# Optimization experiments

Measured on AMD Instinct MI355X. Metric: run time of the kernel, lower is better.

## Reference

```python
import jax, jax.numpy as jnp
import numpy as np

EMBED_DIM = 1024
NUM_HEADS = 16
HEAD_DIM = EMBED_DIM // NUM_HEADS
MLP_HIDDEN = 4096


def layer_norm(x, gamma, beta, eps=1e-5):
    mu = jnp.mean(x, axis=-1, keepdims=True)
    var = jnp.var(x, axis=-1, keepdims=True)
    return (x - mu) / jnp.sqrt(var + eps) * gamma + beta


def setup_inputs() -> dict:
    key = jax.random.key(0)
    ks = jax.random.split(key, 16)
    d, h = EMBED_DIM, MLP_HIDDEN
    s = 0.02
    inp = {
        "x": jax.random.normal(ks[0], (2, 2048, d), dtype=jnp.float32),
        "ln1_g": jnp.ones((d,), jnp.float32),
        "ln1_b": jnp.zeros((d,), jnp.float32),
        "ln2_g": jnp.ones((d,), jnp.float32),
        "ln2_b": jnp.zeros((d,), jnp.float32),
        "Wq": jax.random.normal(ks[1], (d, d), jnp.float32) * s,
        "bq": jnp.zeros((d,), jnp.float32),
        "Wk": jax.random.normal(ks[2], (d, d), jnp.float32) * s,
        "bk": jnp.zeros((d,), jnp.float32),
        "Wv": jax.random.normal(ks[3], (d, d), jnp.float32) * s,
        "bv": jnp.zeros((d,), jnp.float32),
        "Wo": jax.random.normal(ks[4], (d, d), jnp.float32) * s,
        "bo": jnp.zeros((d,), jnp.float32),
        "W1": jax.random.normal(ks[5], (d, h), jnp.float32) * s,
        "b1": jnp.zeros((h,), jnp.float32),
        "W2": jax.random.normal(ks[6], (h, d), jnp.float32) * s,
        "b2": jnp.zeros((d,), jnp.float32),
    }
    return inp


def reference(x, ln1_g, ln1_b, ln2_g, ln2_b, Wq, bq, Wk, bk, Wv, bv, Wo, bo, W1, b1, W2, b2):
    B, T, C = x.shape
    H, Dh = NUM_HEADS, HEAD_DIM
    # attention branch
    xn = layer_norm(x, ln1_g, ln1_b)
    q = (xn @ Wq + bq).reshape(B, T, H, Dh).transpose(0, 2, 1, 3)  # [B,H,T,Dh]
    k = (xn @ Wk + bk).reshape(B, T, H, Dh).transpose(0, 2, 1, 3)
    v = (xn @ Wv + bv).reshape(B, T, H, Dh).transpose(0, 2, 1, 3)
    scores = jnp.einsum('bhtd,bhsd->bhts', q, k) / jnp.sqrt(jnp.float32(Dh))
    attn = jax.nn.softmax(scores, axis=-1)
    out = jnp.einsum('bhts,bhsd->bhtd', attn, v)
    out = out.transpose(0, 2, 1, 3).reshape(B, T, C)
    x = x + out @ Wo + bo
    # MLP branch
    xn2 = layer_norm(x, ln2_g, ln2_b)
    x = x + jax.nn.relu(xn2 @ W1 + b1) @ W2 + b2
    return x
```

## Files before the change

kernel.cpp:

```cpp
#include <hip/hip_runtime.h>

typedef float f32x4 __attribute__((ext_vector_type(4)));
typedef __bf16 bf16x8 __attribute__((ext_vector_type(8)));

constexpr int TT   = 2048;
constexpr int CC   = 1024;
constexpr int HIDN = 4096;
constexpr int MM   = 4096;
constexpr int NQKV = 3072;

union U84 { uint32_t u[4]; bf16x8 v; };

__device__ inline uint32_t cvt_pk_bf16(float lo, float hi) {
  uint32_t r;
  asm("v_cvt_pk_bf16_f32 %0, %1, %2" : "=v"(r) : "v"(lo), "v"(hi));
  return r;
}
__device__ inline ushort f2bf(float f) { return (ushort)(cvt_pk_bf16(f, 0.f) & 0xffffu); }
__device__ inline float bfbits2f(uint32_t bits) {
  union { uint32_t u; float f; } c; c.u = bits; return c.f;
}
__device__ inline float exp2_fast(float x) {
  float r;
  asm("v_exp_f32 %0, %1" : "=v"(r) : "v"(x));
  return r;
}

#define AS1C(p) ((__attribute__((address_space(1))) void*)(p))
#define AS3(p)  ((__attribute__((address_space(3))) void*)(p))

__global__ __launch_bounds__(256) void prep_weights(const float* __restrict__ Wq,
                                                    const float* __restrict__ Wk,
                                                    const float* __restrict__ Wv,
                                                    const float* __restrict__ Wo,
                                                    const float* __restrict__ W1,
                                                    const float* __restrict__ W2,
                                                    const float* __restrict__ bq,
                                                    const float* __restrict__ bk,
                                                    const float* __restrict__ bv,
                                                    const float* __restrict__ x,
                                                    const float* __restrict__ g1,
                                                    const float* __restrict__ b1v,
                                                    ushort* __restrict__ WqkvT,
                                                    ushort* __restrict__ WoT,
                                                    ushort* __restrict__ W1T,
                                                    ushort* __restrict__ W2T,
                                                    float* __restrict__ Bqkv,
                                                    ushort* __restrict__ Xn) {
  const int id = blockIdx.x;
  const int t = threadIdx.x;
  if (id >= 12300) {
    const int row = id - 12300;
    float4 v = reinterpret_cast<const float4*>(x + (size_t)row * CC)[t];
    float s  = v.x + v.y + v.z + v.w;
    float ss = v.x * v.x + v.y * v.y + v.z * v.z + v.w * v.w;
#pragma unroll
    for (int off = 32; off; off >>= 1) {
      s  += __shfl_down(s, off);
      ss += __shfl_down(ss, off);
    }
    __shared__ float red[16];
    const int wid = t >> 6, lane = t & 63;
    if (lane == 0) { red[wid] = s; red[8 + wid] = ss; }
    __syncthreads();
    if (t == 0) {
      red[0] = red[0] + red[1] + red[2] + red[3];
      red[8] = red[8] + red[9] + red[10] + red[11];
    }
    __syncthreads();
    const float mu   = red[0] * (1.0f / CC);
    const float var  = red[8] * (1.0f / CC) - mu * mu;
    const float rstd = rsqrtf(var + 1e-5f);
    float4 gg = reinterpret_cast<const float4*>(g1)[t];
    float4 bb = reinterpret_cast<const float4*>(b1v)[t];
    uint2 st;
    st.x = cvt_pk_bf16((v.x - mu) * rstd * gg.x + bb.x, (v.y - mu) * rstd * gg.y + bb.y);
    st.y = cvt_pk_bf16((v.z - mu) * rstd * gg.z + bb.z, (v.w - mu) * rstd * gg.w + bb.w);
    *reinterpret_cast<uint2*>(Xn + (size_t)row * CC + t * 4) = st;
    return;
  }
  if (id >= 12288) {
    const int i = (id - 12288) * 256 + t;
    Bqkv[i] = (i < 1024) ? bq[i] : ((i < 2048) ? bk[i - 1024] : bv[i - 2048]);
    return;
  }
  const float* W; ushort* out; int Kd, Nd, bx, by, rowOff = 0;
  if (id < 4096) {
    const int which = id >> 10, sub = id & 1023;
    bx = sub & 31; by = sub >> 5; Kd = 1024; Nd = 1024;
    if (which == 0)      { W = Wq; out = WqkvT; rowOff = 0; }
    else if (which == 1) { W = Wk; out = WqkvT; rowOff = 1024; }
    else if (which == 2) { W = Wv; out = WqkvT; rowOff = 2048; }
    else                 { W = Wo; out = WoT; }
  } else if (id < 8192) {
    const int sub = id - 4096; bx = sub & 127; by = sub >> 7;
    W = W1; out = W1T; Kd = 1024; Nd = 4096;
  } else {
    const int sub = id - 8192; bx = sub & 31; by = sub >> 5;
    W = W2; out = W2T; Kd = 4096; Nd = 1024;
  }
  const int n0 = bx * 32, k0 = by * 32;
  __shared__ float Ts[32][33];
  {
    const int r = t >> 3, cb = (t & 7) * 4;
    float4 v = *reinterpret_cast<const float4*>(W + (size_t)(k0 + r) * Nd + n0 + cb);
    Ts[r][cb + 0] = v.x; Ts[r][cb + 1] = v.y; Ts[r][cb + 2] = v.z; Ts[r][cb + 3] = v.w;
  }
  __syncthreads();
  {
    const int nl = t >> 3, kb = (t & 7) * 4;
    uint2 st;
    st.x = cvt_pk_bf16(Ts[kb + 0][nl], Ts[kb + 1][nl]);
    st.y = cvt_pk_bf16(Ts[kb + 2][nl], Ts[kb + 3][nl]);
    *reinterpret_cast<uint2*>(out + (size_t)(rowOff + n0 + nl) * Kd + k0 + kb) = st;
  }
}

template <bool RELU, bool VOUT, bool PARTIAL>
__global__ __launch_bounds__(512, 2) void gemm_8w(const ushort* __restrict__ A,
                                                  const ushort* __restrict__ Bt,
                                                  const float* __restrict__ bias,
                                                  ushort* __restrict__ outp,
                                                  ushort* __restrict__ Vt,
                                                  ushort* __restrict__ P1,
                                                  ushort* __restrict__ P2,
                                                  ushort* __restrict__ P3,
                                                  int N, int K, int Kchunk) {
  __shared__ ushort lds[65536];
  const int t = threadIdx.x, lane = t & 63, w = t >> 6;
  const int g = lane >> 4, i16 = lane & 15;
  const int wr = w >> 2, wc = w & 3;
  const int nwg  = gridDim.x * gridDim.y;
  const int orig = blockIdx.y * gridDim.x + blockIdx.x;
  const int sw   = (orig & 7) * (nwg >> 3) + (orig >> 3);
  const int row0 = (sw / gridDim.x) * 256, col0 = (sw % gridDim.x) * 256;
  const int kstart = PARTIAL ? blockIdx.z * Kchunk : 0;
  const int NT = (PARTIAL ? Kchunk : K) >> 6;
  ushort* __restrict__ Out = outp;
  if (PARTIAL) Out = (blockIdx.z == 0) ? outp : (blockIdx.z == 1) ? P1
              : (blockIdx.z == 2) ? P2 : P3;

  const ushort* aG[4];
  const ushort* bG[4];
#pragma unroll
  for (int i = 0; i < 4; ++i) {
    const int c = t + 512 * i;
    const int r = c >> 3, ssw = (c & 7) ^ (r & 7);
    aG[i] = A  + (size_t)(row0 + r) * K + kstart + ssw * 8;
    bG[i] = Bt + (size_t)(col0 + r) * K + kstart + ssw * 8;
  }

  int aoff[8][2], boff[4][2];
#pragma unroll
  for (int mf = 0; mf < 8; ++mf) {
    const int R = wr * 128 + mf * 16 + i16;
#pragma unroll
    for (int kk = 0; kk < 2; ++kk)
      aoff[mf][kk] = R * 128 + (((kk << 2) | g) ^ (R & 7)) * 16;
  }
#pragma unroll
  for (int nf = 0; nf < 4; ++nf) {
    const int Cn = wc * 64 + nf * 16 + i16;
#pragma unroll
    for (int kk = 0; kk < 2; ++kk)
      boff[nf][kk] = Cn * 128 + (((kk << 2) | g) ^ (Cn & 7)) * 16;
  }

  f32x4 acc[8][4] = {};

  auto STAGE = [&](int bi, int kt) {
    char* aB = (char*)lds + bi * 65536;
    char* bB = aB + 32768;
    const int ko = kt * 64;
#pragma unroll
    for (int i = 0; i < 4; ++i)
      __builtin_amdgcn_global_load_lds(AS1C(aG[i] + ko), AS3(aB + i * 8192 + w * 1024), 16, 0, 0);
#pragma unroll
    for (int i = 0; i < 4; ++i)
      __builtin_amdgcn_global_load_lds(AS1C(bG[i] + ko), AS3(bB + i * 8192 + w * 1024), 16, 0, 0);
  };

  STAGE(0, 0);

  for (int kt = 0; kt < NT; ++kt) {
    const int cur = kt & 1;
    if (kt + 1 < NT) {
      STAGE(cur ^ 1, kt + 1);
      asm volatile("s_waitcnt vmcnt(8)" ::: "memory");
    } else {
      asm volatile("s_waitcnt vmcnt(0)" ::: "memory");
    }
    asm volatile("s_barrier" ::: "memory");
    __builtin_amdgcn_sched_barrier(0);

    const char* aB = (const char*)lds + cur * 65536;
    const char* bB = aB + 32768;
    bf16x8 b4[4][2], a4[4][2];
#pragma unroll
    for (int nf = 0; nf < 4; ++nf)
#pragma unroll
      for (int kk = 0; kk < 2; ++kk)
        b4[nf][kk] = *reinterpret_cast<const bf16x8*>(bB + boff[nf][kk]);
#pragma unroll
    for (int mf = 0; mf < 4; ++mf)
#pragma unroll
      for (int kk = 0; kk < 2; ++kk)
        a4[mf][kk] = *reinterpret_cast<const bf16x8*>(aB + aoff[mf][kk]);
    __builtin_amdgcn_s_setprio(1);
#pragma unroll
    for (int mf = 0; mf < 4; ++mf)
#pragma unroll
      for (int nf = 0; nf < 4; ++nf)
#pragma unroll
        for (int kk = 0; kk < 2; ++kk)
          acc[mf][nf] = __builtin_amdgcn_mfma_f32_16x16x32_bf16(a4[mf][kk], b4[nf][kk], acc[mf][nf], 0, 0, 0);
    __builtin_amdgcn_s_setprio(0);
    asm volatile("s_barrier" ::: "memory");
    __builtin_amdgcn_sched_barrier(0);
#pragma unroll
    for (int mf = 0; mf < 4; ++mf)
#pragma unroll
      for (int kk = 0; kk < 2; ++kk)
        a4[mf][kk] = *reinterpret_cast<const bf16x8*>(aB + aoff[mf + 4][kk]);
    __builtin_amdgcn_s_setprio(1);
#pragma unroll
    for (int mf = 0; mf < 4; ++mf)
#pragma unroll
      for (int nf = 0; nf < 4; ++nf)
#pragma unroll
        for (int kk = 0; kk < 2; ++kk)
          acc[mf + 4][nf] = __builtin_amdgcn_mfma_f32_16x16x32_bf16(a4[mf][kk], b4[nf][kk], acc[mf + 4][nf], 0, 0, 0);
    __builtin_amdgcn_s_setprio(0);
    asm volatile("s_barrier" ::: "memory");
    __builtin_amdgcn_sched_barrier(0);
  }

  const int qcol0 = col0 + wc * 64;

  if (VOUT && qcol0 >= 2048) {
#pragma unroll
    for (int nf = 0; nf < 4; ++nf) {
      const int ncol = qcol0 + nf * 16 + i16;
      const float bb = bias[ncol];
      const int d = ncol - 2048;
      const int hh = d >> 6, dd = d & 63;
#pragma unroll
      for (int mf = 0; mf < 8; ++mf) {
        const int mrow = row0 + wr * 128 + mf * 16 + 4 * g;
        const int bb_ = mrow >> 11, tok = mrow & 2047;
        uint2 st;
        st.x = cvt_pk_bf16(acc[mf][nf][0] + bb, acc[mf][nf][1] + bb);
        st.y = cvt_pk_bf16(acc[mf][nf][2] + bb, acc[mf][nf][3] + bb);
        *reinterpret_cast<uint2*>(Vt + (size_t)((bb_ * 16 + hh) * 64 + dd) * TT + tok) = st;
      }
    }
    return;
  }

  float* Lf = (float*)((char*)lds + w * 4096);
  const int rr2 = lane >> 2, q = lane & 3;
#pragma unroll
  for (int mf = 0; mf < 8; ++mf) {
#pragma unroll
    for (int nf = 0; nf < 4; ++nf)
#pragma unroll
      for (int r = 0; r < 4; ++r) {
        const int row = 4 * g + r;
        Lf[row * 64 + ((16 * nf + i16) ^ ((row & 7) << 2))] = acc[mf][nf][r];
      }
    asm volatile("s_waitcnt lgkmcnt(0)" ::: "memory");
    uint32_t u[8];
#pragma unroll
    for (int j = 0; j < 4; ++j) {
      f32x4 v = *reinterpret_cast<const f32x4*>(Lf + rr2 * 64 + ((q * 16 + 4 * j) ^ ((rr2 & 7) << 2)));
      float e0 = v[0], e1 = v[1], e2 = v[2], e3 = v[3];
      if (!PARTIAL) {
        const float4 b4v = *reinterpret_cast<const float4*>(bias + qcol0 + q * 16 + 4 * j);
        e0 += b4v.x; e1 += b4v.y; e2 += b4v.z; e3 += b4v.w;
        if (RELU) {
          e0 = fmaxf(e0, 0.f); e1 = fmaxf(e1, 0.f);
          e2 = fmaxf(e2, 0.f); e3 = fmaxf(e3, 0.f);
        }
      }
      u[2 * j + 0] = cvt_pk_bf16(e0, e1);
      u[2 * j + 1] = cvt_pk_bf16(e2, e3);
    }
    const int mrow = row0 + wr * 128 + mf * 16 + rr2;
    ushort* orow = Out + (size_t)mrow * N + qcol0 + q * 16;
    uint4 s0; s0.x = u[0]; s0.y = u[1]; s0.z = u[2]; s0.w = u[3];
    uint4 s1; s1.x = u[4]; s1.y = u[5]; s1.z = u[6]; s1.w = u[7];
    *reinterpret_cast<uint4*>(orow) = s0;
    *reinterpret_cast<uint4*>(orow + 8) = s1;
    asm volatile("s_waitcnt lgkmcnt(0)" ::: "memory");
  }
}

__global__ __launch_bounds__(256) void gemm_splitk(const ushort* __restrict__ A,
                                                   const ushort* __restrict__ Bt,
                                                   ushort* __restrict__ P0,
                                                   ushort* __restrict__ P1,
                                                   ushort* __restrict__ P2,
                                                   ushort* __restrict__ P3,
                                                   int N, int K, int Kchunk) {
  __shared__ ushort Smem[8192];
  ushort* Asm = Smem;
  ushort* Bsm = Smem + 4096;
  const int t = threadIdx.x;
  const int lane = t & 63, w = t >> 6;
  const int g = lane >> 4, i16 = lane & 15;
  const int wrow = w >> 1, wcol = w & 1;
  const int nwg  = gridDim.x * gridDim.y;
  const int orig = blockIdx.y * gridDim.x + blockIdx.x;
  const int sw   = (orig & 7) * (nwg >> 3) + (orig >> 3);
  const int row0 = (sw / gridDim.x) * 128, col0 = (sw % gridDim.x) * 128;
  const int kstart = blockIdx.z * Kchunk;
  ushort* __restrict__ P = (blockIdx.z == 0) ? P0 : (blockIdx.z == 1) ? P1
                          : (blockIdx.z == 2) ? P2 : P3;

  f32x4 acc[4][4] = {};

  const int srow = t >> 2, sc = (t & 3) * 8;
  const ushort* aS1 = A + (size_t)(row0 + srow) * K + sc;
  const ushort* aS2 = A + (size_t)(row0 + 64 + srow) * K + sc;
  const ushort* bS1 = Bt + (size_t)(col0 + srow) * K + sc;
  const ushort* bS2 = Bt + (size_t)(col0 + 64 + srow) * K + sc;
  char* aL1 = (char*)Asm + w * 1024;
  char* aL2 = (char*)Asm + 4096 + w * 1024;
  char* bL1 = (char*)Bsm + w * 1024;
  char* bL2 = (char*)Bsm + 4096 + w * 1024;

  for (int k0 = kstart; k0 < kstart + Kchunk; k0 += 32) {
    __syncthreads();
    __builtin_amdgcn_global_load_lds(AS1C(aS1 + k0), AS3(aL1), 16, 0, 0);
    __builtin_amdgcn_global_load_lds(AS1C(aS2 + k0), AS3(aL2), 16, 0, 0);
    __builtin_amdgcn_global_load_lds(AS1C(bS1 + k0), AS3(bL1), 16, 0, 0);
    __builtin_amdgcn_global_load_lds(AS1C(bS2 + k0), AS3(bL2), 16, 0, 0);
    __syncthreads();

    bf16x8 a4[4], b4[4];
#pragma unroll
    for (int mf = 0; mf < 4; ++mf) {
      const int r = wrow * 64 + mf * 16 + i16;
      a4[mf] = *reinterpret_cast<const bf16x8*>((const char*)Asm + r * 64 + g * 16);
    }
#pragma unroll
    for (int nf = 0; nf < 4; ++nf) {
      const int c = wcol * 64 + nf * 16 + i16;
      b4[nf] = *reinterpret_cast<const bf16x8*>((const char*)Bsm + c * 64 + g * 16);
    }
#pragma unroll
    for (int mf = 0; mf < 4; ++mf)
#pragma unroll
      for (int nf = 0; nf < 4; ++nf)
        acc[mf][nf] = __builtin_amdgcn_mfma_f32_16x16x32_bf16(a4[mf], b4[nf], acc[mf][nf], 0, 0, 0);
  }

  __syncthreads();

  float* Lf = (float*)((char*)Smem + w * 4096);
  const int qcol0 = col0 + wcol * 64;
  const int rr = lane >> 2, q = lane & 3;
#pragma unroll
  for (int mf = 0; mf < 4; ++mf) {
#pragma unroll
    for (int nf = 0; nf < 4; ++nf)
#pragma unroll
      for (int r = 0; r < 4; ++r) {
        const int row = 4 * g + r;
        Lf[row * 64 + ((16 * nf + i16) ^ ((row & 7) << 2))] = acc[mf][nf][r];
      }
    asm volatile("s_waitcnt lgkmcnt(0)" ::: "memory");
    uint32_t u[8];
#pragma unroll
    for (int j = 0; j < 4; ++j) {
      f32x4 v = *reinterpret_cast<const f32x4*>(Lf + rr * 64 + ((q * 16 + 4 * j) ^ ((rr & 7) << 2)));
      u[2 * j + 0] = cvt_pk_bf16(v[0], v[1]);
      u[2 * j + 1] = cvt_pk_bf16(v[2], v[3]);
    }
    const int mrow = row0 + wrow * 64 + mf * 16 + rr;
    ushort* orow = P + (size_t)mrow * N + qcol0 + q * 16;
    uint4 s0; s0.x = u[0]; s0.y = u[1]; s0.z = u[2]; s0.w = u[3];
    uint4 s1; s1.x = u[4]; s1.y = u[5]; s1.z = u[6]; s1.w = u[7];
    *reinterpret_cast<uint4*>(orow) = s0;
    *reinterpret_cast<uint4*>(orow + 8) = s1;
    asm volatile("s_waitcnt lgkmcnt(0)" ::: "memory");
  }
}

__device__ inline float bfsum4(uint32_t a, uint32_t b, uint32_t c, uint32_t d, bool hi) {
  if (hi) return bfbits2f(a & 0xffff0000u) + bfbits2f(b & 0xffff0000u) +
                 bfbits2f(c & 0xffff0000u) + bfbits2f(d & 0xffff0000u);
  return bfbits2f(a << 16) + bfbits2f(b << 16) + bfbits2f(c << 16) + bfbits2f(d << 16);
}

__global__ __launch_bounds__(256) void reduce_wo_ln(const ushort* __restrict__ P0,
                                                    const ushort* __restrict__ P1,
                                                    const ushort* __restrict__ P2,
                                                    const ushort* __restrict__ P3,
                                                    const float* __restrict__ x,
                                                    const float* __restrict__ bo,
                                                    const float* __restrict__ g,
                                                    const float* __restrict__ b,
                                                    float* __restrict__ X1f,
                                                    ushort* __restrict__ Xn) {
  const int row = blockIdx.x, t = threadIdx.x;
  const size_t off = (size_t)row * CC + t * 4;
  float4 v  = *reinterpret_cast<const float4*>(x + off);
  const uint2 q0 = *reinterpret_cast<const uint2*>(P0 + off);
  const uint2 q1 = *reinterpret_cast<const uint2*>(P1 + off);
  const uint2 q2 = *reinterpret_cast<const uint2*>(P2 + off);
  const uint2 q3 = *reinterpret_cast<const uint2*>(P3 + off);
  float4 bb = reinterpret_cast<const float4*>(bo)[t];
  v.x += bfsum4(q0.x, q1.x, q2.x, q3.x, false) + bb.x;
  v.y += bfsum4(q0.x, q1.x, q2.x, q3.x, true)  + bb.y;
  v.z += bfsum4(q0.y, q1.y, q2.y, q3.y, false) + bb.z;
  v.w += bfsum4(q0.y, q1.y, q2.y, q3.y, true)  + bb.w;
  *reinterpret_cast<float4*>(X1f + off) = v;

  float s  = v.x + v.y + v.z + v.w;
  float ss = v.x * v.x + v.y * v.y + v.z * v.z + v.w * v.w;
#pragma unroll
  for (int o = 32; o; o >>= 1) {
    s  += __shfl_down(s, o);
    ss += __shfl_down(ss, o);
  }
  __shared__ float red[16];
  const int wid = t >> 6, lane = t & 63;
  if (lane == 0) { red[wid] = s; red[8 + wid] = ss; }
  __syncthreads();
  if (t == 0) {
    red[0] = red[0] + red[1] + red[2] + red[3];
    red[8] = red[8] + red[9] + red[10] + red[11];
  }
  __syncthreads();
  const float mu   = red[0] * (1.0f / CC);
  const float var  = red[8] * (1.0f / CC) - mu * mu;
  const float rstd = rsqrtf(var + 1e-5f);
  float4 gg = reinterpret_cast<const float4*>(g)[t];
  float4 lb = reinterpret_cast<const float4*>(b)[t];
  uint2 st;
  st.x = cvt_pk_bf16((v.x - mu) * rstd * gg.x + lb.x, (v.y - mu) * rstd * gg.y + lb.y);
  st.y = cvt_pk_bf16((v.z - mu) * rstd * gg.z + lb.z, (v.w - mu) * rstd * gg.w + lb.w);
  *reinterpret_cast<uint2*>(Xn + off) = st;
}

__global__ __launch_bounds__(256) void reduce_fc2(const ushort* __restrict__ P0,
                                                  const ushort* __restrict__ P1,
                                                  const ushort* __restrict__ P2,
                                                  const ushort* __restrict__ P3,
                                                  const float* __restrict__ X1,
                                                  const float* __restrict__ b2,
                                                  float* __restrict__ out) {
  const int row = blockIdx.x, t = threadIdx.x;
  const size_t off = (size_t)row * CC + t * 4;
  float4 v  = *reinterpret_cast<const float4*>(X1 + off);
  const uint2 q0 = *reinterpret_cast<const uint2*>(P0 + off);
  const uint2 q1 = *reinterpret_cast<const uint2*>(P1 + off);
  const uint2 q2 = *reinterpret_cast<const uint2*>(P2 + off);
  const uint2 q3 = *reinterpret_cast<const uint2*>(P3 + off);
  float4 bb = reinterpret_cast<const float4*>(b2)[t];
  v.x += bfsum4(q0.x, q1.x, q2.x, q3.x, false) + bb.x;
  v.y += bfsum4(q0.x, q1.x, q2.x, q3.x, true)  + bb.y;
  v.z += bfsum4(q0.y, q1.y, q2.y, q3.y, false) + bb.z;
  v.w += bfsum4(q0.y, q1.y, q2.y, q3.y, true)  + bb.w;
  *reinterpret_cast<float4*>(out + off) = v;
}

__global__ __launch_bounds__(512, 4) void attn_full(const ushort* __restrict__ qkv,
                                                    const ushort* __restrict__ Vt,
                                                    ushort* __restrict__ attnb) {
  __shared__ ushort Ks[2][4096];
  __shared__ ushort Vs[2][4096];
  __shared__ uint32_t Ps[8][16][36];
  const int t = threadIdx.x, lane = t & 63, w = t >> 6;
  const int g = lane >> 4, iq = lane & 15;
  const int flat = blockIdx.x;
  const int work = (flat & 7) * 64 + (flat >> 3);
  const int bh = work >> 4;
  const int qt = work & 15;
  const int b = bh >> 4, h = bh & 15;

  bf16x8 qfrag[2];
  {
    const ushort* qrow = qkv + (size_t)(b * TT + qt * 128 + w * 16 + iq) * NQKV + h * 64;
    const float qs = 0.125f * 1.44269504f;
#pragma unroll
    for (int kk = 0; kk < 2; ++kk) {
      uint4 raw = *reinterpret_cast<const uint4*>(qrow + kk * 32 + g * 8);
      uint32_t rr[4] = {raw.x, raw.y, raw.z, raw.w};
      U84 tmp;
#pragma unroll
      for (int c = 0; c < 4; ++c) {
        float lo = bfbits2f(rr[c] << 16) * qs;
        float hi = bfbits2f(rr[c] & 0xffff0000u) * qs;
        tmp.u[c] = cvt_pk_bf16(lo, hi);
      }
      qfrag[kk] = tmp.v;
    }
  }

  const int sr1 = t >> 3, sc1 = t & 7;
  const int csw = (sc1 ^ (sr1 & 7)) * 8;
  const ushort* kbase = qkv + 1024 + h * 64;
  const ushort* vbase = Vt + (size_t)(bh * 64) * TT;

  auto STAGE = [&](int bi, int kt) {
    const size_t tok = (size_t)(b * TT + kt * 64);
    __builtin_amdgcn_global_load_lds(AS1C(kbase + (tok + sr1) * NQKV + csw),
                                     AS3((char*)&Ks[bi][0] + w * 1024), 16, 0, 0);
    __builtin_amdgcn_global_load_lds(AS1C(vbase + (size_t)sr1 * TT + kt * 64 + csw),
                                     AS3((char*)&Vs[bi][0] + w * 1024), 16, 0, 0);
  };

  uint32_t (*pw)[36] = Ps[w];
  const int wsw = (iq & 8) << 1;
  const int xsb = wsw << 2;
  const char* prow = (const char*)&pw[iq][0];

  float lrun = 0.f;
  f32x4 ot[4] = {};

  constexpr int NKT = TT / 64;
  STAGE(0, 0);

  for (int kt = 0; kt < NKT; ++kt) {
    const int cur = kt & 1;
    if (kt + 1 < NKT) {
      STAGE(cur ^ 1, kt + 1);
      asm volatile("s_waitcnt vmcnt(2)" ::: "memory");
    } else {
      asm volatile("s_waitcnt vmcnt(0)" ::: "memory");
    }
    asm volatile("s_barrier" ::: "memory");
    __builtin_amdgcn_sched_barrier(0);
    const char* Kc = (const char*)&Ks[cur][0];
    const char* Vc = (const char*)&Vs[cur][0];

    f32x4 sfr[4] = {};
    __builtin_amdgcn_s_setprio(1);
#pragma unroll
    for (int kk = 0; kk < 2; ++kk)
#pragma unroll
      for (int jf = 0; jf < 4; ++jf) {
        const int row = iq + 16 * jf;
        const int off = row * 128 + ((kk * 64 + g * 16) ^ ((row & 7) << 4));
        bf16x8 a = *reinterpret_cast<const bf16x8*>(Kc + off);
        sfr[jf] = __builtin_amdgcn_mfma_f32_16x16x32_bf16(a, qfrag[kk], sfr[jf], 0, 0, 0);
      }
    __builtin_amdgcn_s_setprio(0);

#pragma unroll
    for (int f = 0; f < 4; ++f) {
      float p0 = exp2_fast(sfr[f][0]);
      float p1 = exp2_fast(sfr[f][1]);
      float p2 = exp2_fast(sfr[f][2]);
      float p3 = exp2_fast(sfr[f][3]);
      lrun += (p0 + p1) + (p2 + p3);
      uint2 st2;
      st2.x = cvt_pk_bf16(p0, p1);
      st2.y = cvt_pk_bf16(p2, p3);
      *reinterpret_cast<uint2*>(&pw[iq][(8 * f + 2 * g) ^ wsw]) = st2;
    }
    asm volatile("s_waitcnt lgkmcnt(0)" ::: "memory");

    __builtin_amdgcn_s_setprio(1);
#pragma unroll
    for (int kk = 0; kk < 2; ++kk) {
      bf16x8 pb = *reinterpret_cast<const bf16x8*>(prow + ((kk * 64 + g * 16) ^ xsb));
#pragma unroll
      for (int df = 0; df < 4; ++df) {
        const int row = iq + 16 * df;
        const int off = row * 128 + ((kk * 64 + g * 16) ^ ((row & 7) << 4));
        bf16x8 a = *reinterpret_cast<const bf16x8*>(Vc + off);
        ot[df] = __builtin_amdgcn_mfma_f32_16x16x32_bf16(a, pb, ot[df], 0, 0, 0);
      }
    }
    __builtin_amdgcn_s_setprio(0);

    asm volatile("s_barrier" ::: "memory");
    __builtin_amdgcn_sched_barrier(0);
  }

  lrun += __shfl_xor(lrun, 16, 64);
  lrun += __shfl_xor(lrun, 32, 64);
  const int grow = b * TT + qt * 128 + w * 16 + iq;
  const float inv = 1.f / lrun;
  ushort* orow = attnb + (size_t)grow * CC + h * 64;
#pragma unroll
  for (int df = 0; df < 4; ++df) {
    uint2 st;
    st.x = cvt_pk_bf16(ot[df][0] * inv, ot[df][1] * inv);
    st.y = cvt_pk_bf16(ot[df][2] * inv, ot[df][3] * inv);
    *reinterpret_cast<uint2*>(orow + df * 16 + g * 4) = st;
  }
}

extern "C" void kernel_launch(void* const* d_in, const int* in_sizes, int n_in,
                              void* d_out, int out_size, void* d_ws, size_t ws_size,
                              hipStream_t stream) {
  const float* x     = (const float*)d_in[0];
  const float* ln1_g = (const float*)d_in[1];
  const float* ln1_b = (const float*)d_in[2];
  const float* ln2_g = (const float*)d_in[3];
  const float* ln2_b = (const float*)d_in[4];
  const float* Wq = (const float*)d_in[5];
  const float* bq = (const float*)d_in[6];
  const float* Wk = (const float*)d_in[7];
  const float* bk = (const float*)d_in[8];
  const float* Wv = (const float*)d_in[9];
  const float* bv = (const float*)d_in[10];
  const float* Wo = (const float*)d_in[11];
  const float* bo = (const float*)d_in[12];
  const float* W1 = (const float*)d_in[13];
  const float* b1 = (const float*)d_in[14];
  const float* W2 = (const float*)d_in[15];
  const float* b2 = (const float*)d_in[16];
  float* out = (float*)d_out;
  char* ws = (char*)d_ws;

  ushort* WqkvT = (ushort*)(ws + 0);
  ushort* WoT   = (ushort*)(ws + 6291456);
  ushort* W1T   = (ushort*)(ws + 8388608);
  ushort* W2T   = (ushort*)(ws + 16777216);
  float*  Bqkv  = (float*) (ws + 25165824);
  ushort* Xn    = (ushort*)(ws + 25178112);
  ushort* Attn  = (ushort*)(ws + 33566720);
  float*  X1f   = (float*) (ws + 41955328);
  ushort* Qkv   = (ushort*)(ws + 58732544);
  ushort* Vtb   = (ushort*)(ws + 83898368);
  ushort* Hid   = (ushort*)(ws + 58732544);
  ushort* WoP0  = (ushort*)(ws + 58732544);
  ushort* WoP1  = (ushort*)(ws + 67121152);
  ushort* WoP2  = (ushort*)(ws + 75509760);
  ushort* WoP3  = (ushort*)(ws + 83898368);
  ushort* F2P0  = (ushort*)(ws + 0);
  ushort* F2P1  = (ushort*)(ws + 8388608);
  ushort* F2P2  = (ushort*)(ws + 25178112);
  ushort* F2P3  = (ushort*)(ws + 33566720);

  const dim3 blk(256);

  prep_weights<<<dim3(16396), blk, 0, stream>>>(Wq, Wk, Wv, Wo, W1, W2, bq, bk, bv,
                                                x, ln1_g, ln1_b,
                                                WqkvT, WoT, W1T, W2T, Bqkv, Xn);
  gemm_8w<false, true, false><<<dim3(12, 16), dim3(512), 0, stream>>>(
      Xn, WqkvT, Bqkv, Qkv, Vtb, nullptr, nullptr, nullptr, NQKV, 1024, 0);
  attn_full<<<dim3(512), dim3(512), 0, stream>>>(Qkv, Vtb, Attn);
  gemm_splitk<<<dim3(8, 32, 4), blk, 0, stream>>>(Attn, WoT, WoP0, WoP1, WoP2, WoP3, 1024, 1024, 256);
  reduce_wo_ln<<<dim3(MM), blk, 0, stream>>>(WoP0, WoP1, WoP2, WoP3, x, bo, ln2_g, ln2_b, X1f, Xn);
  gemm_8w<true, false, false><<<dim3(16, 16), dim3(512), 0, stream>>>(
      Xn, W1T, b1, Hid, nullptr, nullptr, nullptr, nullptr, HIDN, 1024, 0);
  gemm_8w<false, false, true><<<dim3(4, 16, 4), dim3(512), 0, stream>>>(
      Hid, W2T, nullptr, F2P0, nullptr, F2P1, F2P2, F2P3, 1024, 4096, 1024);
  reduce_fc2<<<dim3(MM), blk, 0, stream>>>(F2P0, F2P1, F2P2, F2P3, X1f, b2, out);
}
```

Measured before the change: 234.4 us.

## Split attention over two KV halves with a combine kernel; reuse gemm_8w for Wo

The attention kernel now splits each (batch, head, query-tile) across two halves of the key sequence. This doubles the grid to 1024 workgroups for better CU fill. Each half writes an unnormalized bf16 partial output plus its row sums, and a new combine kernel adds the two partials and normalizes. The Wo projection drops its dedicated 256-thread split-K GEMM and uses the existing 8-wave gemm_8w split-K path. The trade-off is an extra kernel launch, extra memory traffic for the partials, and bf16 rounding of unnormalized partials. The combine also assumes both halves share the same max offset, since no per-half max is stored or rescaled.

Result: no change. 236.1 us (+0.8%).

```diff
diff --git a/kernel.cpp b/kernel.cpp
--- a/kernel.cpp
+++ b/kernel.cpp
@@ -295,98 +295,6 @@
   }
 }
 
-__global__ __launch_bounds__(256) void gemm_splitk(const ushort* __restrict__ A,
-                                                   const ushort* __restrict__ Bt,
-                                                   ushort* __restrict__ P0,
-                                                   ushort* __restrict__ P1,
-                                                   ushort* __restrict__ P2,
-                                                   ushort* __restrict__ P3,
-                                                   int N, int K, int Kchunk) {
-  __shared__ ushort Smem[8192];
-  ushort* Asm = Smem;
-  ushort* Bsm = Smem + 4096;
-  const int t = threadIdx.x;
-  const int lane = t & 63, w = t >> 6;
-  const int g = lane >> 4, i16 = lane & 15;
-  const int wrow = w >> 1, wcol = w & 1;
-  const int nwg  = gridDim.x * gridDim.y;
-  const int orig = blockIdx.y * gridDim.x + blockIdx.x;
-  const int sw   = (orig & 7) * (nwg >> 3) + (orig >> 3);
-  const int row0 = (sw / gridDim.x) * 128, col0 = (sw % gridDim.x) * 128;
-  const int kstart = blockIdx.z * Kchunk;
-  ushort* __restrict__ P = (blockIdx.z == 0) ? P0 : (blockIdx.z == 1) ? P1
-                          : (blockIdx.z == 2) ? P2 : P3;
-
-  f32x4 acc[4][4] = {};
-
-  const int srow = t >> 2, sc = (t & 3) * 8;
-  const ushort* aS1 = A + (size_t)(row0 + srow) * K + sc;
-  const ushort* aS2 = A + (size_t)(row0 + 64 + srow) * K + sc;
-  const ushort* bS1 = Bt + (size_t)(col0 + srow) * K + sc;
-  const ushort* bS2 = Bt + (size_t)(col0 + 64 + srow) * K + sc;
-  char* aL1 = (char*)Asm + w * 1024;
-  char* aL2 = (char*)Asm + 4096 + w * 1024;
-  char* bL1 = (char*)Bsm + w * 1024;
-  char* bL2 = (char*)Bsm + 4096 + w * 1024;
-
-  for (int k0 = kstart; k0 < kstart + Kchunk; k0 += 32) {
-    __syncthreads();
-    __builtin_amdgcn_global_load_lds(AS1C(aS1 + k0), AS3(aL1), 16, 0, 0);
-    __builtin_amdgcn_global_load_lds(AS1C(aS2 + k0), AS3(aL2), 16, 0, 0);
-    __builtin_amdgcn_global_load_lds(AS1C(bS1 + k0), AS3(bL1), 16, 0, 0);
-    __builtin_amdgcn_global_load_lds(AS1C(bS2 + k0), AS3(bL2), 16, 0, 0);
-    __syncthreads();
-
-    bf16x8 a4[4], b4[4];
-#pragma unroll
-    for (int mf = 0; mf < 4; ++mf) {
-      const int r = wrow * 64 + mf * 16 + i16;
-      a4[mf] = *reinterpret_cast<const bf16x8*>((const char*)Asm + r * 64 + g * 16);
-    }
-#pragma unroll
-    for (int nf = 0; nf < 4; ++nf) {
-      const int c = wcol * 64 + nf * 16 + i16;
-      b4[nf] = *reinterpret_cast<const bf16x8*>((const char*)Bsm + c * 64 + g * 16);
-    }
-#pragma unroll
-    for (int mf = 0; mf < 4; ++mf)
-#pragma unroll
-      for (int nf = 0; nf < 4; ++nf)
-        acc[mf][nf] = __builtin_amdgcn_mfma_f32_16x16x32_bf16(a4[mf], b4[nf], acc[mf][nf], 0, 0, 0);
-  }
-
-  __syncthreads();
-
-  float* Lf = (float*)((char*)Smem + w * 4096);
-  const int qcol0 = col0 + wcol * 64;
-  const int rr = lane >> 2, q = lane & 3;
-#pragma unroll
-  for (int mf = 0; mf < 4; ++mf) {
-#pragma unroll
-    for (int nf = 0; nf < 4; ++nf)
-#pragma unroll
-      for (int r = 0; r < 4; ++r) {
-        const int row = 4 * g + r;
-        Lf[row * 64 + ((16 * nf + i16) ^ ((row & 7) << 2))] = acc[mf][nf][r];
-      }
-    asm volatile("s_waitcnt lgkmcnt(0)" ::: "memory");
-    uint32_t u[8];
-#pragma unroll
-    for (int j = 0; j < 4; ++j) {
-      f32x4 v = *reinterpret_cast<const f32x4*>(Lf + rr * 64 + ((q * 16 + 4 * j) ^ ((rr & 7) << 2)));
-      u[2 * j + 0] = cvt_pk_bf16(v[0], v[1]);
-      u[2 * j + 1] = cvt_pk_bf16(v[2], v[3]);
-    }
-    const int mrow = row0 + wrow * 64 + mf * 16 + rr;
-    ushort* orow = P + (size_t)mrow * N + qcol0 + q * 16;
-    uint4 s0; s0.x = u[0]; s0.y = u[1]; s0.z = u[2]; s0.w = u[3];
-    uint4 s1; s1.x = u[4]; s1.y = u[5]; s1.z = u[6]; s1.w = u[7];
-    *reinterpret_cast<uint4*>(orow) = s0;
-    *reinterpret_cast<uint4*>(orow + 8) = s1;
-    asm volatile("s_waitcnt lgkmcnt(0)" ::: "memory");
-  }
-}
-
 __device__ inline float bfsum4(uint32_t a, uint32_t b, uint32_t c, uint32_t d, bool hi) {
   if (hi) return bfbits2f(a & 0xffff0000u) + bfbits2f(b & 0xffff0000u) +
                  bfbits2f(c & 0xffff0000u) + bfbits2f(d & 0xffff0000u);
@@ -466,19 +374,24 @@
   *reinterpret_cast<float4*>(out + off) = v;
 }
 
-__global__ __launch_bounds__(512, 4) void attn_full(const ushort* __restrict__ qkv,
-                                                    const ushort* __restrict__ Vt,
-                                                    ushort* __restrict__ attnb) {
+__global__ __launch_bounds__(512, 4) void attn_partial(const ushort* __restrict__ qkv,
+                                                       const ushort* __restrict__ Vt,
+                                                       ushort* __restrict__ O0,
+                                                       ushort* __restrict__ O1,
+                                                       float* __restrict__ lbuf) {
   __shared__ ushort Ks[2][4096];
   __shared__ ushort Vs[2][4096];
   __shared__ uint32_t Ps[8][16][36];
   const int t = threadIdx.x, lane = t & 63, w = t >> 6;
   const int g = lane >> 4, iq = lane & 15;
   const int flat = blockIdx.x;
-  const int work = (flat & 7) * 64 + (flat >> 3);
-  const int bh = work >> 4;
-  const int qt = work & 15;
+  const int work = (flat & 7) * 128 + (flat >> 3);
+  const int bh = work >> 5;
+  const int rem = work & 31;
+  const int z = rem >> 4;
+  const int qt = rem & 15;
   const int b = bh >> 4, h = bh & 15;
+  ushort* __restrict__ Obuf = z ? O1 : O0;
 
   bf16x8 qfrag[2];
   {
@@ -520,12 +433,12 @@
   float lrun = 0.f;
   f32x4 ot[4] = {};
 
-  constexpr int NKT = TT / 64;
-  STAGE(0, 0);
-
-  for (int kt = 0; kt < NKT; ++kt) {
+  const int kt0 = z * 16, ktE = kt0 + 16;
+  STAGE(0, kt0);
+
+  for (int kt = kt0; kt < ktE; ++kt) {
     const int cur = kt & 1;
-    if (kt + 1 < NKT) {
+    if (kt + 1 < ktE) {
       STAGE(cur ^ 1, kt + 1);
       asm volatile("s_waitcnt vmcnt(2)" ::: "memory");
     } else {
@@ -584,15 +497,38 @@
   lrun += __shfl_xor(lrun, 16, 64);
   lrun += __shfl_xor(lrun, 32, 64);
   const int grow = b * TT + qt * 128 + w * 16 + iq;
-  const float inv = 1.f / lrun;
-  ushort* orow = attnb + (size_t)grow * CC + h * 64;
+  ushort* orow = Obuf + (size_t)grow * CC + h * 64;
 #pragma unroll
   for (int df = 0; df < 4; ++df) {
     uint2 st;
-    st.x = cvt_pk_bf16(ot[df][0] * inv, ot[df][1] * inv);
-    st.y = cvt_pk_bf16(ot[df][2] * inv, ot[df][3] * inv);
+    st.x = cvt_pk_bf16(ot[df][0], ot[df][1]);
+    st.y = cvt_pk_bf16(ot[df][2], ot[df][3]);
     *reinterpret_cast<uint2*>(orow + df * 16 + g * 4) = st;
   }
+  if (g == 0 && (lane >> 4) == 0)
+    lbuf[(size_t)z * (MM * 16) + (size_t)grow * 16 + h] = lrun;
+}
+
+__global__ __launch_bounds__(256) void attn_combine(const ushort* __restrict__ O0,
+                                                    const ushort* __restrict__ O1,
+                                                    const float* __restrict__ lbuf,
+                                                    ushort* __restrict__ attnb) {
+  const int row = blockIdx.x, t = threadIdx.x;
+  const int h = t >> 4;
+  const float l0 = lbuf[(size_t)row * 16 + h];
+  const float l1 = lbuf[(size_t)MM * 16 + (size_t)row * 16 + h];
+  const float inv = 1.f / (l0 + l1);
+  const size_t off = (size_t)row * CC + t * 4;
+  const uint2 r0 = *reinterpret_cast<const uint2*>(O0 + off);
+  const uint2 r1 = *reinterpret_cast<const uint2*>(O1 + off);
+  const float o0 = (bfbits2f(r0.x << 16)         + bfbits2f(r1.x << 16))         * inv;
+  const float o1 = (bfbits2f(r0.x & 0xffff0000u) + bfbits2f(r1.x & 0xffff0000u)) * inv;
+  const float o2 = (bfbits2f(r0.y << 16)         + bfbits2f(r1.y << 16))         * inv;
+  const float o3 = (bfbits2f(r0.y & 0xffff0000u) + bfbits2f(r1.y & 0xffff0000u)) * inv;
+  uint2 st;
+  st.x = cvt_pk_bf16(o0, o1);
+  st.y = cvt_pk_bf16(o2, o3);
+  *reinterpret_cast<uint2*>(attnb + off) = st;
 }
 
 extern "C" void kernel_launch(void* const* d_in, const int* in_sizes, int n_in,
@@ -629,6 +565,9 @@
   ushort* Qkv   = (ushort*)(ws + 58732544);
   ushort* Vtb   = (ushort*)(ws + 83898368);
   ushort* Hid   = (ushort*)(ws + 58732544);
+  ushort* OP0   = (ushort*)(ws + 41955328);
+  ushort* OP1   = (ushort*)(ws + 50343936);
+  float*  lbuf  = (float*) (ws + 0);
   ushort* WoP0  = (ushort*)(ws + 58732544);
   ushort* WoP1  = (ushort*)(ws + 67121152);
   ushort* WoP2  = (ushort*)(ws + 75509760);
@@ -645,8 +584,10 @@
                                                 WqkvT, WoT, W1T, W2T, Bqkv, Xn);
   gemm_8w<false, true, false><<<dim3(12, 16), dim3(512), 0, stream>>>(
       Xn, WqkvT, Bqkv, Qkv, Vtb, nullptr, nullptr, nullptr, NQKV, 1024, 0);
-  attn_full<<<dim3(512), dim3(512), 0, stream>>>(Qkv, Vtb, Attn);
-  gemm_splitk<<<dim3(8, 32, 4), blk, 0, stream>>>(Attn, WoT, WoP0, WoP1, WoP2, WoP3, 1024, 1024, 256);
+  attn_partial<<<dim3(1024), dim3(512), 0, stream>>>(Qkv, Vtb, OP0, OP1, lbuf);
+  attn_combine<<<dim3(MM), blk, 0, stream>>>(OP0, OP1, lbuf, Attn);
+  gemm_8w<false, false, true><<<dim3(4, 16, 4), dim3(512), 0, stream>>>(
+      Attn, WoT, nullptr, WoP0, nullptr, WoP1, WoP2, WoP3, 1024, 1024, 256);
   reduce_wo_ln<<<dim3(MM), blk, 0, stream>>>(WoP0, WoP1, WoP2, WoP3, x, bo, ln2_g, ln2_b, X1f, Xn);
   gemm_8w<true, false, false><<<dim3(16, 16), dim3(512), 0, stream>>>(
       Xn, W1T, b1, Hid, nullptr, nullptr, nullptr, nullptr, HIDN, 1024, 0);
```
